# Performance work log

Measured on AMD Instinct MI355X. Metric: run time of the kernel, lower is better.

Reference implementation:

```python
import jax, jax.numpy as jnp
import numpy as np

N, D, H = 524288, 3, 64

def setup_inputs() -> dict:
    key = jax.random.key(0)
    ks = jax.random.split(key, 7)
    s1 = 1.0 / np.sqrt(D)
    s2 = 1.0 / np.sqrt(H)
    return {
        "x":  jax.random.normal(ks[0], (N, D), dtype=jnp.float32),
        "W1": jax.random.normal(ks[1], (H, D), dtype=jnp.float32) * s1,
        "b1": jax.random.normal(ks[2], (H,),   dtype=jnp.float32) * s1,
        "W2": jax.random.normal(ks[3], (H, H), dtype=jnp.float32) * s2,
        "b2": jax.random.normal(ks[4], (H,),   dtype=jnp.float32) * s2,
        "W3": jax.random.normal(ks[5], (D, H), dtype=jnp.float32) * s2,
        "b3": jax.random.normal(ks[6], (D,),   dtype=jnp.float32) * s2,
    }

def reference(x, W1, b1, W2, b2, W3, b3):
    # psi: 2-hidden-layer tanh MLP, R^3 -> R^3 (vector potential).
    h1 = jnp.tanh(x @ W1.T + b1)            # (N, H)
    h2 = jnp.tanh(h1 @ W2.T + b2)           # (N, H)
    # Analytic Jacobian J[n, i, j] = d psi_i / d x_j via forward-mode chain rule
    # (equivalent to the d autograd.grad calls in the torch module).
    D1 = 1.0 - h1 * h1                      # tanh' at layer 1, (N, H)
    D2 = 1.0 - h2 * h2                      # tanh' at layer 2, (N, H)
    T1 = D1[:, :, None] * W1                # (N, H, d): d h1 / d x
    T2 = D2[:, :, None] * jnp.einsum('hk,nkd->nhd', W2, T1)  # (N, H, d): d h2 / d x
    J = jnp.einsum('ih,nhd->nid', W3, T2)   # (N, d, d)
    # curl psi for d = 3
    curl = jnp.stack(
        (J[:, 2, 1] - J[:, 1, 2],
         J[:, 0, 2] - J[:, 2, 0],
         J[:, 1, 0] - J[:, 0, 1]), axis=-1)  # (N, 3)
    return curl
```

## Files before the change

kernel.cpp:

```cpp
#include <hip/hip_runtime.h>

typedef __attribute__((ext_vector_type(8))) _Float16 f16x8;
typedef __attribute__((ext_vector_type(2))) __fp16 fp16x2r;
typedef __attribute__((ext_vector_type(4))) float f32x4;
typedef __attribute__((ext_vector_type(2))) float f32x2;

#define BLK   256
#define NWAVE 4
#define NPT   16
#define MAXB  2048

union F16U  { uint4 u; f16x8 v; };
union PairU { float4 f4; f32x2 p[2]; };
union AccU  { f32x4 v; f32x2 p[2]; };

__device__ __forceinline__ f32x2 pk_fma(f32x2 a, f32x2 b, f32x2 c) {
    return __builtin_elementwise_fma(a, b, c);
}
__device__ __forceinline__ f32x2 pk_mul(f32x2 a, f32x2 b) { return a * b; }
__device__ __forceinline__ f32x2 pk_add(f32x2 a, f32x2 b) { return a + b; }

__device__ __forceinline__ f32x2 tanh2(f32x2 a, f32x2 cst2, f32x2 one2, f32x2 ntwo2) {
    f32x2 earg = pk_mul(a, cst2);
    f32x2 e;
    e.x = __builtin_amdgcn_exp2f(earg.x);
    e.y = __builtin_amdgcn_exp2f(earg.y);
    f32x2 ep1 = pk_add(e, one2);
    f32x2 r;
    r.x = __builtin_amdgcn_rcpf(ep1.x);
    r.y = __builtin_amdgcn_rcpf(ep1.y);
    return pk_fma(ntwo2, r, one2);
}

__device__ __forceinline__ unsigned int pkh(float a, float b) {
    union { fp16x2r h; unsigned int u; } t;
    t.h = __builtin_amdgcn_cvt_pkrtz(a, b);
    return t.u;
}

__device__ __forceinline__ f16x8 pack8h(const float* v) {
    F16U r;
    r.u = make_uint4(pkh(v[0], v[1]), pkh(v[2], v[3]),
                     pkh(v[4], v[5]), pkh(v[6], v[7]));
    return r.v;
}

#define MFMA __builtin_amdgcn_mfma_f32_16x16x32_f16

__global__ __launch_bounds__(BLK, 2) void curl_mfma(
    const float* __restrict__ x,  const float* __restrict__ W1,
    const float* __restrict__ b1, const float* __restrict__ W2,
    const float* __restrict__ b2, const float* __restrict__ W3,
    float* __restrict__ out, int npts, int iters, int ntiles)
{
    __shared__ uint4  sA[8 * 64];
    __shared__ float4 sW1xy[32], sW1zb[32];
    __shared__ float4 sLUTa[32], sLUTb[32];

    const int tid  = threadIdx.x;
    const int wv   = tid >> 6;
    const int lane = tid & 63;
    const int p    = lane & 15;
    const int q    = lane >> 4;

    if (tid < 32) {
        {
            const int qq = tid >> 3, kc = (tid >> 2) & 1, u = tid & 3;
            const int k0 = qq * 16 + kc * 8 + u * 2, k1 = k0 + 1;
            const int slot = ((kc * 4 + u) << 2) | qq;
            sW1xy[slot] = make_float4(W1[k0*3+0], W1[k1*3+0], W1[k0*3+1], W1[k1*3+1]);
            sW1zb[slot] = make_float4(W1[k0*3+2], W1[k1*3+2], b1[k0],     b1[k1]);
        }
        {
            const int m = tid >> 3, qq = (tid >> 1) & 3, rp = tid & 1;
            const int h0 = m * 16 + qq * 4 + rp * 2, h1 = h0 + 1;
            sLUTa[tid] = make_float4(b2[h0], b2[h1], W3[h0], W3[h1]);
            sLUTb[tid] = make_float4(W3[64+h0], W3[64+h1], W3[128+h0], W3[128+h1]);
        }
    }

    {
        const int m = wv;
#pragma unroll
        for (int kc = 0; kc < 2; ++kc) {
            const float* src = W2 + (m * 16 + p) * 64 + q * 16 + kc * 8;
            const float4 va = ((const float4*)src)[0];
            const float4 vb = ((const float4*)src)[1];
            const float vv[8] = {va.x, va.y, va.z, va.w, vb.x, vb.y, vb.z, vb.w};
            F16U uh; uh.v = pack8h(vv);
            sA[(m * 2 + kc) * 64 + lane] = uh.u;
        }
    }
    __syncthreads();

    const f32x2 one2  = {1.0f, 1.0f};
    const f32x2 none2 = {-1.0f, -1.0f};
    const f32x2 ntwo2 = {-2.0f, -2.0f};
    const f32x2 cst2  = {2.8853900817779268f, 2.8853900817779268f};

    const int gw = blockIdx.x * NWAVE + wv;
    const int nw = gridDim.x * NWAVE;

    for (int it = 0; it < iters; ++it) {
        const int tile = gw + it * nw;
        if (tile >= ntiles) break;
        const int id = tile * NPT + p;

        float x0 = 0.f, x1 = 0.f, x2 = 0.f;
        if (id < npts) {
            x0 = x[id * 3 + 0];
            x1 = x[id * 3 + 1];
            x2 = x[id * 3 + 2];
        }
        const f32x2 x0_2 = {x0, x0}, x1_2 = {x1, x1}, x2_2 = {x2, x2};

        f16x8 Bf[4][2];
#pragma unroll
        for (int kc = 0; kc < 2; ++kc) {
            unsigned int wh[4], w0[4], w1[4], w2[4];
#pragma unroll
            for (int u = 0; u < 4; ++u) {
                PairU wxy, wzb;
                wxy.f4 = sW1xy[((kc * 4 + u) << 2) | q];
                wzb.f4 = sW1zb[((kc * 4 + u) << 2) | q];
                f32x2 a = pk_fma(wxy.p[0], x0_2, wzb.p[1]);
                a = pk_fma(wxy.p[1], x1_2, a);
                a = pk_fma(wzb.p[0], x2_2, a);
                const f32x2 th = tanh2(a, cst2, one2, ntwo2);
                const f32x2 t2 = pk_mul(th, th);
                const f32x2 d1 = pk_fma(t2, none2, one2);
                const f32x2 g0 = pk_mul(d1, wxy.p[0]);
                const f32x2 g1 = pk_mul(d1, wxy.p[1]);
                const f32x2 g2 = pk_mul(d1, wzb.p[0]);
                wh[u] = pkh(th.x, th.y);
                w0[u] = pkh(g0.x, g0.y);
                w1[u] = pkh(g1.x, g1.y);
                w2[u] = pkh(g2.x, g2.y);
            }
            F16U t;
            t.u = make_uint4(wh[0], wh[1], wh[2], wh[3]); Bf[0][kc] = t.v;
            t.u = make_uint4(w0[0], w0[1], w0[2], w0[3]); Bf[1][kc] = t.v;
            t.u = make_uint4(w1[0], w1[1], w1[2], w1[3]); Bf[2][kc] = t.v;
            t.u = make_uint4(w2[0], w2[1], w2[2], w2[3]); Bf[3][kc] = t.v;
        }

        f32x2 cp0 = {0.f,0.f}, cp1 = cp0, cp2 = cp0;
        f32x2 cn0 = cp0, cn1 = cp0, cn2 = cp0;
#pragma unroll 1
        for (int m = 0; m < 4; ++m) {
            F16U A0, A1;
            const uint4* pA = &sA[(m * 2) * 64 + lane];
            A0.u = pA[0];
            A1.u = pA[64];

            AccU a0, a1, a2, a3;
            a0.v = (f32x4){0.f,0.f,0.f,0.f}; a1.v = a0.v; a2.v = a0.v; a3.v = a0.v;
            a0.v = MFMA(A0.v, Bf[0][0], a0.v, 0, 0, 0);
            a1.v = MFMA(A0.v, Bf[1][0], a1.v, 0, 0, 0);
            a2.v = MFMA(A0.v, Bf[2][0], a2.v, 0, 0, 0);
            a3.v = MFMA(A0.v, Bf[3][0], a3.v, 0, 0, 0);
            a0.v = MFMA(A1.v, Bf[0][1], a0.v, 0, 0, 0);
            a1.v = MFMA(A1.v, Bf[1][1], a1.v, 0, 0, 0);
            a2.v = MFMA(A1.v, Bf[2][1], a2.v, 0, 0, 0);
            a3.v = MFMA(A1.v, Bf[3][1], a3.v, 0, 0, 0);

#pragma unroll
            for (int rp = 0; rp < 2; ++rp) {
                PairU la, lb;
                la.f4 = sLUTa[m * 8 + q * 2 + rp];
                lb.f4 = sLUTb[m * 8 + q * 2 + rp];
                const f32x2 s0 = pk_add(a0.p[rp], la.p[0]);
                const f32x2 th = tanh2(s0, cst2, one2, ntwo2);
                const f32x2 t2 = pk_mul(th, th);
                const f32x2 d2 = pk_fma(t2, none2, one2);
                const f32x2 e0 = pk_mul(la.p[1], d2);
                const f32x2 e1 = pk_mul(lb.p[0], d2);
                const f32x2 e2 = pk_mul(lb.p[1], d2);
                cp0 = pk_fma(e2, a2.p[rp], cp0);  cn0 = pk_fma(e1, a3.p[rp], cn0);
                cp1 = pk_fma(e0, a3.p[rp], cp1);  cn1 = pk_fma(e2, a1.p[rp], cn1);
                cp2 = pk_fma(e1, a1.p[rp], cp2);  cn2 = pk_fma(e0, a2.p[rp], cn2);
            }
        }

        float c0 = (cp0.x - cn0.x) + (cp0.y - cn0.y);
        float c1 = (cp1.x - cn1.x) + (cp1.y - cn1.y);
        float c2 = (cp2.x - cn2.x) + (cp2.y - cn2.y);

        c0 += __shfl_xor(c0, 16); c0 += __shfl_xor(c0, 32);
        c1 += __shfl_xor(c1, 16); c1 += __shfl_xor(c1, 32);
        c2 += __shfl_xor(c2, 16); c2 += __shfl_xor(c2, 32);

        if (q < 3 && id < npts) {
            const float cv = (q == 0) ? c0 : ((q == 1) ? c1 : c2);
            out[tile * (NPT * 3) + p * 3 + q] = cv;
        }
    }
}

extern "C" void kernel_launch(void* const* d_in, const int* in_sizes, int n_in,
                              void* d_out, int out_size, void* d_ws, size_t ws_size,
                              hipStream_t stream) {
    const float* x  = (const float*)d_in[0];
    const float* W1 = (const float*)d_in[1];
    const float* b1 = (const float*)d_in[2];
    const float* W2 = (const float*)d_in[3];
    const float* b2 = (const float*)d_in[4];
    const float* W3 = (const float*)d_in[5];
    float* out = (float*)d_out;

    const int npts   = in_sizes[0] / 3;
    const int ntiles = (npts + NPT - 1) / NPT;
    int blocks = (ntiles + NWAVE - 1) / NWAVE;
    if (blocks > MAXB) blocks = MAXB;
    const int nw    = blocks * NWAVE;
    const int iters = (ntiles + nw - 1) / nw;

    hipLaunchKernelGGL(curl_mfma, dim3(blocks), dim3(BLK), 0, stream,
                       x, W1, b1, W2, b2, W3, out, npts, iters, ntiles);
}
```

Measured before the change: 104.1 us.

## Software-pipeline tiles: prefetch x and compute next layer-1 B fragments during MFMA

Restructures the per-wave tile loop into a two-stage software pipeline with double-buffered B fragments. The next tile's x is prefetched two tiles ahead, and its layer-1 tanh/gradient fragments are computed before the current tile's MFMA and layer-2 stage runs. The aim is to hide global load latency and interleave VALU work with MFMA work. The cost is more live registers (two Bf sets), which could cause spilling or lower occupancy under launch_bounds(256,2).

```diff
diff --git a/kernel.cpp b/kernel.cpp
--- a/kernel.cpp
+++ b/kernel.cpp
@@ -20,7 +20,10 @@
 __device__ __forceinline__ f32x2 pk_mul(f32x2 a, f32x2 b) { return a * b; }
 __device__ __forceinline__ f32x2 pk_add(f32x2 a, f32x2 b) { return a + b; }
 
-__device__ __forceinline__ f32x2 tanh2(f32x2 a, f32x2 cst2, f32x2 one2, f32x2 ntwo2) {
+__device__ __forceinline__ f32x2 tanh2(f32x2 a) {
+    const f32x2 one2  = {1.0f, 1.0f};
+    const f32x2 ntwo2 = {-2.0f, -2.0f};
+    const f32x2 cst2  = {2.8853900817779268f, 2.8853900817779268f};
     f32x2 earg = pk_mul(a, cst2);
     f32x2 e;
     e.x = __builtin_amdgcn_exp2f(earg.x);
@@ -47,6 +50,103 @@
 
 #define MFMA __builtin_amdgcn_mfma_f32_16x16x32_f16
 
+__device__ __forceinline__ void computeB(
+    float x0, float x1, float x2,
+    const float4* sW1xy, const float4* sW1zb, int q, f16x8 (&Bf)[4][2])
+{
+    const f32x2 one2  = {1.0f, 1.0f};
+    const f32x2 none2 = {-1.0f, -1.0f};
+    const f32x2 x0_2 = {x0, x0}, x1_2 = {x1, x1}, x2_2 = {x2, x2};
+#pragma unroll
+    for (int kc = 0; kc < 2; ++kc) {
+        unsigned int wh[4], w0[4], w1[4], w2[4];
+#pragma unroll
+        for (int u = 0; u < 4; ++u) {
+            PairU wxy, wzb;
+            wxy.f4 = sW1xy[((kc * 4 + u) << 2) | q];
+            wzb.f4 = sW1zb[((kc * 4 + u) << 2) | q];
+            f32x2 a = pk_fma(wxy.p[0], x0_2, wzb.p[1]);
+            a = pk_fma(wxy.p[1], x1_2, a);
+            a = pk_fma(wzb.p[0], x2_2, a);
+            const f32x2 th = tanh2(a);
+            const f32x2 t2 = pk_mul(th, th);
+            const f32x2 d1 = pk_fma(t2, none2, one2);
+            const f32x2 g0 = pk_mul(d1, wxy.p[0]);
+            const f32x2 g1 = pk_mul(d1, wxy.p[1]);
+            const f32x2 g2 = pk_mul(d1, wzb.p[0]);
+            wh[u] = pkh(th.x, th.y);
+            w0[u] = pkh(g0.x, g0.y);
+            w1[u] = pkh(g1.x, g1.y);
+            w2[u] = pkh(g2.x, g2.y);
+        }
+        F16U t;
+        t.u = make_uint4(wh[0], wh[1], wh[2], wh[3]); Bf[0][kc] = t.v;
+        t.u = make_uint4(w0[0], w0[1], w0[2], w0[3]); Bf[1][kc] = t.v;
+        t.u = make_uint4(w1[0], w1[1], w1[2], w1[3]); Bf[2][kc] = t.v;
+        t.u = make_uint4(w2[0], w2[1], w2[2], w2[3]); Bf[3][kc] = t.v;
+    }
+}
+
+__device__ __forceinline__ void processTile(
+    const f16x8 (&Bf)[4][2], const uint4* sA,
+    const float4* sLUTa, const float4* sLUTb,
+    int lane, int q, int p, int tile, int npts, float* __restrict__ out)
+{
+    const f32x2 one2  = {1.0f, 1.0f};
+    const f32x2 none2 = {-1.0f, -1.0f};
+    f32x2 cp0 = {0.f,0.f}, cp1 = cp0, cp2 = cp0;
+    f32x2 cn0 = cp0, cn1 = cp0, cn2 = cp0;
+#pragma unroll 1
+    for (int m = 0; m < 4; ++m) {
+        F16U A0, A1;
+        const uint4* pA = &sA[(m * 2) * 64 + lane];
+        A0.u = pA[0];
+        A1.u = pA[64];
+
+        AccU a0, a1, a2, a3;
+        a0.v = (f32x4){0.f,0.f,0.f,0.f}; a1.v = a0.v; a2.v = a0.v; a3.v = a0.v;
+        a0.v = MFMA(A0.v, Bf[0][0], a0.v, 0, 0, 0);
+        a1.v = MFMA(A0.v, Bf[1][0], a1.v, 0, 0, 0);
+        a2.v = MFMA(A0.v, Bf[2][0], a2.v, 0, 0, 0);
+        a3.v = MFMA(A0.v, Bf[3][0], a3.v, 0, 0, 0);
+        a0.v = MFMA(A1.v, Bf[0][1], a0.v, 0, 0, 0);
+        a1.v = MFMA(A1.v, Bf[1][1], a1.v, 0, 0, 0);
+        a2.v = MFMA(A1.v, Bf[2][1], a2.v, 0, 0, 0);
+        a3.v = MFMA(A1.v, Bf[3][1], a3.v, 0, 0, 0);
+
+#pragma unroll
+        for (int rp = 0; rp < 2; ++rp) {
+            PairU la, lb;
+            la.f4 = sLUTa[m * 8 + q * 2 + rp];
+            lb.f4 = sLUTb[m * 8 + q * 2 + rp];
+            const f32x2 s0 = pk_add(a0.p[rp], la.p[0]);
+            const f32x2 th = tanh2(s0);
+            const f32x2 t2 = pk_mul(th, th);
+            const f32x2 d2 = pk_fma(t2, none2, one2);
+            const f32x2 e0 = pk_mul(la.p[1], d2);
+            const f32x2 e1 = pk_mul(lb.p[0], d2);
+            const f32x2 e2 = pk_mul(lb.p[1], d2);
+            cp0 = pk_fma(e2, a2.p[rp], cp0);  cn0 = pk_fma(e1, a3.p[rp], cn0);
+            cp1 = pk_fma(e0, a3.p[rp], cp1);  cn1 = pk_fma(e2, a1.p[rp], cn1);
+            cp2 = pk_fma(e1, a1.p[rp], cp2);  cn2 = pk_fma(e0, a2.p[rp], cn2);
+        }
+    }
+
+    float c0 = (cp0.x - cn0.x) + (cp0.y - cn0.y);
+    float c1 = (cp1.x - cn1.x) + (cp1.y - cn1.y);
+    float c2 = (cp2.x - cn2.x) + (cp2.y - cn2.y);
+
+    c0 += __shfl_xor(c0, 16); c0 += __shfl_xor(c0, 32);
+    c1 += __shfl_xor(c1, 16); c1 += __shfl_xor(c1, 32);
+    c2 += __shfl_xor(c2, 16); c2 += __shfl_xor(c2, 32);
+
+    const int id = tile * NPT + p;
+    if (q < 3 && id < npts) {
+        const float cv = (q == 0) ? c0 : ((q == 1) ? c1 : c2);
+        out[tile * (NPT * 3) + p * 3 + q] = cv;
+    }
+}
+
 __global__ __launch_bounds__(BLK, 2) void curl_mfma(
     const float* __restrict__ x,  const float* __restrict__ W1,
     const float* __restrict__ b1, const float* __restrict__ W2,
@@ -93,107 +193,44 @@
     }
     __syncthreads();
 
-    const f32x2 one2  = {1.0f, 1.0f};
-    const f32x2 none2 = {-1.0f, -1.0f};
-    const f32x2 ntwo2 = {-2.0f, -2.0f};
-    const f32x2 cst2  = {2.8853900817779268f, 2.8853900817779268f};
-
     const int gw = blockIdx.x * NWAVE + wv;
     const int nw = gridDim.x * NWAVE;
 
-    for (int it = 0; it < iters; ++it) {
-        const int tile = gw + it * nw;
-        if (tile >= ntiles) break;
-        const int id = tile * NPT + p;
-
-        float x0 = 0.f, x1 = 0.f, x2 = 0.f;
-        if (id < npts) {
-            x0 = x[id * 3 + 0];
-            x1 = x[id * 3 + 1];
-            x2 = x[id * 3 + 2];
-        }
-        const f32x2 x0_2 = {x0, x0}, x1_2 = {x1, x1}, x2_2 = {x2, x2};
-
-        f16x8 Bf[4][2];
-#pragma unroll
-        for (int kc = 0; kc < 2; ++kc) {
-            unsigned int wh[4], w0[4], w1[4], w2[4];
-#pragma unroll
-            for (int u = 0; u < 4; ++u) {
-                PairU wxy, wzb;
-                wxy.f4 = sW1xy[((kc * 4 + u) << 2) | q];
-                wzb.f4 = sW1zb[((kc * 4 + u) << 2) | q];
-                f32x2 a = pk_fma(wxy.p[0], x0_2, wzb.p[1]);
-                a = pk_fma(wxy.p[1], x1_2, a);
-                a = pk_fma(wzb.p[0], x2_2, a);
-                const f32x2 th = tanh2(a, cst2, one2, ntwo2);
-                const f32x2 t2 = pk_mul(th, th);
-                const f32x2 d1 = pk_fma(t2, none2, one2);
-                const f32x2 g0 = pk_mul(d1, wxy.p[0]);
-                const f32x2 g1 = pk_mul(d1, wxy.p[1]);
-                const f32x2 g2 = pk_mul(d1, wzb.p[0]);
-                wh[u] = pkh(th.x, th.y);
-                w0[u] = pkh(g0.x, g0.y);
-                w1[u] = pkh(g1.x, g1.y);
-                w2[u] = pkh(g2.x, g2.y);
+    auto loadx = [&](int t, float& a, float& b, float& c) {
+        a = 0.f; b = 0.f; c = 0.f;
+        if (t < ntiles) {
+            const int idn = t * NPT + p;
+            if (idn < npts) {
+                a = x[idn * 3 + 0];
+                b = x[idn * 3 + 1];
+                c = x[idn * 3 + 2];
             }
-            F16U t;
-            t.u = make_uint4(wh[0], wh[1], wh[2], wh[3]); Bf[0][kc] = t.v;
-            t.u = make_uint4(w0[0], w0[1], w0[2], w0[3]); Bf[1][kc] = t.v;
-            t.u = make_uint4(w1[0], w1[1], w1[2], w1[3]); Bf[2][kc] = t.v;
-            t.u = make_uint4(w2[0], w2[1], w2[2], w2[3]); Bf[3][kc] = t.v;
-        }
-
-        f32x2 cp0 = {0.f,0.f}, cp1 = cp0, cp2 = cp0;
-        f32x2 cn0 = cp0, cn1 = cp0, cn2 = cp0;
-#pragma unroll 1
-        for (int m = 0; m < 4; ++m) {
-            F16U A0, A1;
-            const uint4* pA = &sA[(m * 2) * 64 + lane];
-            A0.u = pA[0];
-            A1.u = pA[64];
-
-            AccU a0, a1, a2, a3;
-            a0.v = (f32x4){0.f,0.f,0.f,0.f}; a1.v = a0.v; a2.v = a0.v; a3.v = a0.v;
-            a0.v = MFMA(A0.v, Bf[0][0], a0.v, 0, 0, 0);
-            a1.v = MFMA(A0.v, Bf[1][0], a1.v, 0, 0, 0);
-            a2.v = MFMA(A0.v, Bf[2][0], a2.v, 0, 0, 0);
-            a3.v = MFMA(A0.v, Bf[3][0], a3.v, 0, 0, 0);
-            a0.v = MFMA(A1.v, Bf[0][1], a0.v, 0, 0, 0);
-            a1.v = MFMA(A1.v, Bf[1][1], a1.v, 0, 0, 0);
-            a2.v = MFMA(A1.v, Bf[2][1], a2.v, 0, 0, 0);
-            a3.v = MFMA(A1.v, Bf[3][1], a3.v, 0, 0, 0);
-
-#pragma unroll
-            for (int rp = 0; rp < 2; ++rp) {
-                PairU la, lb;
-                la.f4 = sLUTa[m * 8 + q * 2 + rp];
-                lb.f4 = sLUTb[m * 8 + q * 2 + rp];
-                const f32x2 s0 = pk_add(a0.p[rp], la.p[0]);
-                const f32x2 th = tanh2(s0, cst2, one2, ntwo2);
-                const f32x2 t2 = pk_mul(th, th);
-                const f32x2 d2 = pk_fma(t2, none2, one2);
-                const f32x2 e0 = pk_mul(la.p[1], d2);
-                const f32x2 e1 = pk_mul(lb.p[0], d2);
-                const f32x2 e2 = pk_mul(lb.p[1], d2);
-                cp0 = pk_fma(e2, a2.p[rp], cp0);  cn0 = pk_fma(e1, a3.p[rp], cn0);
-                cp1 = pk_fma(e0, a3.p[rp], cp1);  cn1 = pk_fma(e2, a1.p[rp], cn1);
-                cp2 = pk_fma(e1, a1.p[rp], cp2);  cn2 = pk_fma(e0, a2.p[rp], cn2);
-            }
-        }
-
-        float c0 = (cp0.x - cn0.x) + (cp0.y - cn0.y);
-        float c1 = (cp1.x - cn1.x) + (cp1.y - cn1.y);
-        float c2 = (cp2.x - cn2.x) + (cp2.y - cn2.y);
-
-        c0 += __shfl_xor(c0, 16); c0 += __shfl_xor(c0, 32);
-        c1 += __shfl_xor(c1, 16); c1 += __shfl_xor(c1, 32);
-        c2 += __shfl_xor(c2, 16); c2 += __shfl_xor(c2, 32);
-
-        if (q < 3 && id < npts) {
-            const float cv = (q == 0) ? c0 : ((q == 1) ? c1 : c2);
-            out[tile * (NPT * 3) + p * 3 + q] = cv;
-        }
+        }
+    };
+
+    float xb0, xb1, xb2, xc0, xc1, xc2;
+    f16x8 BfA[4][2], BfB[4][2];
+
+    {
+        float xa0, xa1, xa2;
+        loadx(gw, xa0, xa1, xa2);
+        loadx(gw + nw, xb0, xb1, xb2);
+        computeB(xa0, xa1, xa2, sW1xy, sW1zb, q, BfA);
+    }
+
+    for (int it = 0; it < iters; it += 2) {
+        const int tA = gw + it * nw;
+        if (tA >= ntiles) break;
+        const int tB = tA + nw;
+
+        loadx(tA + 2 * nw, xc0, xc1, xc2);
+        computeB(xb0, xb1, xb2, sW1xy, sW1zb, q, BfB);
+        processTile(BfA, sA, sLUTa, sLUTb, lane, q, p, tA, npts, out);
+
+        loadx(tA + 3 * nw, xb0, xb1, xb2);
+        if (tB >= ntiles) break;
+        computeB(xc0, xc1, xc2, sW1xy, sW1zb, q, BfA);
+        processTile(BfB, sA, sLUTa, sLUTb, lane, q, p, tB, npts, out);
     }
 }
 
```

New measurement: 104.7 us. About the same (+0.6%).
